# Optimization experiments

Measured on AMD Instinct MI355X. Metric: run time of the kernel, lower is better.

The kernel has to match this reference:

```python
import jax, jax.numpy as jnp
import numpy as np

N = 50000   # nodes
E = 800000  # edges (avg degree 16)
IN = 128
H = 128
OUT = 16
BN_EPS = 1e-5


def _uniform(key, shape, fan_in):
    s = 1.0 / np.sqrt(fan_in)
    return jax.random.uniform(key, shape, jnp.float32, -s, s)


def setup_inputs() -> dict:
    key = jax.random.key(0)
    ks = jax.random.split(key, 12)
    x = jax.random.normal(ks[0], (N, IN), jnp.float32)
    edge_index = jax.random.randint(ks[1], (2, E), 0, N, dtype=jnp.int64)
    # SAGEConv layer 1: lin_l (with bias) on aggregated neighbors, lin_r (no bias) on root
    Wl1 = _uniform(ks[2], (H, IN), IN)
    bl1 = _uniform(ks[3], (H,), IN)
    Wr1 = _uniform(ks[4], (H, IN), IN)
    # SAGEConv layer 2
    Wl2 = _uniform(ks[5], (OUT, H), H)
    bl2 = _uniform(ks[6], (OUT,), H)
    Wr2 = _uniform(ks[7], (OUT, H), H)
    # BatchNorm1d(H) affine params
    gamma = jnp.ones((H,), jnp.float32)
    beta = jnp.zeros((H,), jnp.float32)
    # PReLU single shared slope
    a = jnp.array(0.25, jnp.float32)
    return {"x": x, "edge_index": edge_index, "Wl1": Wl1, "bl1": bl1, "Wr1": Wr1,
            "Wl2": Wl2, "bl2": bl2, "Wr2": Wr2, "gamma": gamma, "beta": beta, "a": a}


def sage_conv(x, src, dst, Wl, bl, Wr):
    # mean-aggregate source features at destination nodes
    msg = x[src]                                              # [E, F] gather
    summ = jax.ops.segment_sum(msg, dst, num_segments=N)      # [N, F] scatter-add
    cnt = jax.ops.segment_sum(jnp.ones((src.shape[0],), x.dtype), dst, num_segments=N)
    agg = summ / jnp.clip(cnt, 1.0)[:, None]
    return agg @ Wl.T + bl + x @ Wr.T


def reference(x, edge_index, Wl1, bl1, Wr1, Wl2, bl2, Wr2, gamma, beta, a):
    src, dst = edge_index[0], edge_index[1]
    # layer 1: SAGEConv -> BatchNorm (batch stats) -> PReLU -> residual
    h = sage_conv(x, src, dst, Wl1, bl1, Wr1)
    mean = h.mean(axis=0)
    var = h.var(axis=0)  # biased, as in torch BN training
    h = gamma * (h - mean) / jnp.sqrt(var + BN_EPS) + beta
    h = jnp.where(h >= 0, h, a * h)  # PReLU (shared slope)
    h = h + x  # residual (hidden == in)
    # layer 2 + log_softmax over classes
    out = sage_conv(h, src, dst, Wl2, bl2, Wr2)
    return jax.nn.log_softmax(out, axis=1)
```

## Files before the change

### kernel.cpp

```cpp
#include <hip/hip_runtime.h>

#define NNODES 50000
#define EEDGES 800000
#define FIN 128
#define FH 128
#define FOUT 16
#define BN_EPS 1e-5f
#define NBIN 391
#define CAP 4096
#define PCH 2048
#define NPB 391
#define NTILES 1563
#define PACKBLKS 3143

typedef short bf16x8 __attribute__((ext_vector_type(8)));
typedef float f32x4 __attribute__((ext_vector_type(4)));

__device__ inline unsigned short tobf16(float f) {
    unsigned int u = __float_as_uint(f);
    u += 0x7fffu + ((u >> 16) & 1u);
    return (unsigned short)(u >> 16);
}
__device__ inline float frombf16(unsigned short h) {
    return __uint_as_float(((unsigned int)h) << 16);
}
__device__ inline unsigned packbf(float f0, float f1) {
    return (unsigned)tobf16(f0) | ((unsigned)tobf16(f1) << 16);
}
__device__ inline float lo16(unsigned u) { return __uint_as_float(u << 16); }
__device__ inline float hi16(unsigned u) { return __uint_as_float(u & 0xffff0000u); }

__global__ void zero_kernel(int* __restrict__ p) {
    for (int i = threadIdx.x; i < 647; i += 256) p[i] = 0;
}

__global__ void part_pack_kernel(const int* __restrict__ src, const int* __restrict__ dst,
                                 int* __restrict__ binFill, unsigned int* __restrict__ edgeBin,
                                 const float* __restrict__ x,
                                 const float* __restrict__ Wl1, const float* __restrict__ Wr1,
                                 const float* __restrict__ Wl2, const float* __restrict__ Wr2,
                                 unsigned short* __restrict__ xb, unsigned short* __restrict__ wb) {
    __shared__ int hist[NBIN];
    __shared__ int runBase[NBIN];
    __shared__ int runFill[NBIN];
    int t = threadIdx.x;
    if (blockIdx.x < NPB) {
        for (int i = t; i < NBIN; i += 256) { hist[i] = 0; runFill[i] = 0; }
        __syncthreads();
        int e0 = blockIdx.x * PCH;
        for (int i = 0; i < PCH / 256; ++i) {
            int e = e0 + i * 256 + t;
            if (e < EEDGES) atomicAdd(&hist[dst[e] >> 7], 1);
        }
        __syncthreads();
        for (int i = t; i < NBIN; i += 256) {
            int c = hist[i];
            if (c) runBase[i] = atomicAdd(&binFill[i], c);
        }
        __syncthreads();
        for (int i = 0; i < PCH / 256; ++i) {
            int e = e0 + i * 256 + t;
            if (e < EEDGES) {
                int d = dst[e];
                int b = d >> 7;
                int off = runBase[b] + atomicAdd(&runFill[b], 1);
                if (off < CAP)
                    edgeBin[(size_t)b * CAP + off] = ((unsigned)(d & 127) << 17) | (unsigned)src[e];
            }
        }
    } else {
        int tt = (blockIdx.x - NPB) * 256 + t;
        int base = tt * 8;
        const float* srcp;
        unsigned short* dstp;
        int off;
        if (base < NNODES * FIN) {
            srcp = x; off = base; dstp = xb + base;
        } else {
            int w = base - NNODES * FIN;
            if (w >= 36864) return;
            dstp = wb + w;
            if (w < 16384)      { srcp = Wl1; off = w; }
            else if (w < 32768) { srcp = Wr1; off = w - 16384; }
            else if (w < 34816) { srcp = Wl2; off = w - 32768; }
            else                { srcp = Wr2; off = w - 34816; }
        }
        float4 f0 = *reinterpret_cast<const float4*>(srcp + off);
        float4 f1 = *reinterpret_cast<const float4*>(srcp + off + 4);
        uint4 r;
        r.x = packbf(f0.x, f0.y);
        r.y = packbf(f0.z, f0.w);
        r.z = packbf(f1.x, f1.y);
        r.w = packbf(f1.z, f1.w);
        *reinterpret_cast<uint4*>(dstp) = r;
    }
}

__global__ void bucket_fused_kernel(const unsigned int* __restrict__ edgeBin,
                                    const int* __restrict__ binFill,
                                    int* __restrict__ srcSorted,
                                    int* __restrict__ rowstart) {
    __shared__ unsigned eb[CAP];
    __shared__ int cnt[128];
    __shared__ int sc[128];
    __shared__ int wp[128];
    __shared__ int wsum[4];
    int b = blockIdx.x;
    int t = threadIdx.x;

    int contrib = 0;
    if (t < NBIN && t < b) contrib += binFill[t];
    int t2 = t + 256;
    if (t2 < NBIN && t2 < b) contrib += binFill[t2];
    for (int off = 32; off; off >>= 1) contrib += __shfl_down(contrib, off, 64);
    if ((t & 63) == 0) wsum[t >> 6] = contrib;
    if (t < 128) cnt[t] = 0;
    __syncthreads();
    int binOffB = wsum[0] + wsum[1] + wsum[2] + wsum[3];

    int n = min(binFill[b], CAP);
    for (int k = t; k < n; k += 256) {
        unsigned c = edgeBin[(size_t)b * CAP + k];
        eb[k] = c;
        atomicAdd(&cnt[c >> 17], 1);
    }
    __syncthreads();

    if (t < 128) sc[t] = cnt[t];
    __syncthreads();
    for (int off = 1; off < 128; off <<= 1) {
        int v = (t < 128 && t >= off) ? sc[t - off] : 0;
        __syncthreads();
        if (t < 128) sc[t] += v;
        __syncthreads();
    }
    if (t < 128) {
        int node = b * 128 + t;
        int rs = binOffB + sc[t] - cnt[t];
        wp[t] = rs;
        if (node < NNODES) rowstart[node] = rs;
    }
    if (b == 0 && t == 128) rowstart[NNODES] = EEDGES;
    __syncthreads();

    for (int k = t; k < n; k += 256) {
        unsigned c = eb[k];
        int p = atomicAdd(&wp[c >> 17], 1);
        srcSorted[p] = (int)(c & 0x1FFFF);
    }
}

__global__ void gather_bf16(const unsigned short* __restrict__ feat,
                            const int* __restrict__ rowstart,
                            const int* __restrict__ srcSorted,
                            unsigned short* __restrict__ aggout) {
    int tid = threadIdx.x;
    int i = blockIdx.x * 4 + (tid >> 6);
    int j = tid & 63;
    const unsigned int* fp = (const unsigned int*)feat;
    int k0 = rowstart[i], k1 = rowstart[i + 1];
    float a0 = 0.0f, a1 = 0.0f;
    int k = k0;
    for (; k + 8 <= k1; k += 8) {
        int s0 = srcSorted[k],     s1 = srcSorted[k + 1], s2 = srcSorted[k + 2], s3 = srcSorted[k + 3];
        int s4 = srcSorted[k + 4], s5 = srcSorted[k + 5], s6 = srcSorted[k + 6], s7 = srcSorted[k + 7];
        unsigned int u0 = fp[(size_t)s0 * 64 + j];
        unsigned int u1 = fp[(size_t)s1 * 64 + j];
        unsigned int u2 = fp[(size_t)s2 * 64 + j];
        unsigned int u3 = fp[(size_t)s3 * 64 + j];
        unsigned int u4 = fp[(size_t)s4 * 64 + j];
        unsigned int u5 = fp[(size_t)s5 * 64 + j];
        unsigned int u6 = fp[(size_t)s6 * 64 + j];
        unsigned int u7 = fp[(size_t)s7 * 64 + j];
        a0 += lo16(u0) + lo16(u1) + lo16(u2) + lo16(u3) + lo16(u4) + lo16(u5) + lo16(u6) + lo16(u7);
        a1 += hi16(u0) + hi16(u1) + hi16(u2) + hi16(u3) + hi16(u4) + hi16(u5) + hi16(u6) + hi16(u7);
    }
    for (; k + 4 <= k1; k += 4) {
        int s0 = srcSorted[k], s1 = srcSorted[k + 1], s2 = srcSorted[k + 2], s3 = srcSorted[k + 3];
        unsigned int u0 = fp[(size_t)s0 * 64 + j];
        unsigned int u1 = fp[(size_t)s1 * 64 + j];
        unsigned int u2 = fp[(size_t)s2 * 64 + j];
        unsigned int u3 = fp[(size_t)s3 * 64 + j];
        a0 += lo16(u0) + lo16(u1) + lo16(u2) + lo16(u3);
        a1 += hi16(u0) + hi16(u1) + hi16(u2) + hi16(u3);
    }
    for (; k < k1; ++k) {
        unsigned int u = fp[(size_t)srcSorted[k] * 64 + j];
        a0 += lo16(u);
        a1 += hi16(u);
    }
    float inv = 1.0f / (float)max(k1 - k0, 1);
    ((unsigned int*)aggout)[(size_t)i * 64 + j] = packbf(a0 * inv, a1 * inv);
}

__global__ void __launch_bounds__(256, 2)
lin1_persist(const unsigned short* __restrict__ aggb,
             const unsigned short* __restrict__ xb,
             const unsigned short* __restrict__ wl,
             const unsigned short* __restrict__ wr,
             const float* __restrict__ bias,
             unsigned short* __restrict__ hb,
             float* __restrict__ bnsum, float* __restrict__ bnsq) {
    __shared__ float bps[128];
    __shared__ float bpq[128];
    int tid = threadIdx.x;
    if (tid < 128) { bps[tid] = 0.0f; bpq[tid] = 0.0f; }
    __syncthreads();
    int wave = tid >> 6;
    int lane = tid & 63;
    int c = wave & 1;
    int rsub = wave >> 1;
    int lrow = lane & 15;
    int kg = lane >> 4;

    bf16x8 wlF[4][4], wrF[4][4];
    #pragma unroll
    for (int nf = 0; nf < 4; ++nf) {
        #pragma unroll
        for (int ks = 0; ks < 4; ++ks) {
            wlF[nf][ks] = *(const bf16x8*)(wl + (size_t)(c * 64 + nf * 16 + lrow) * 128 + ks * 32 + kg * 8);
            wrF[nf][ks] = *(const bf16x8*)(wr + (size_t)(c * 64 + nf * 16 + lrow) * 128 + ks * 32 + kg * 8);
        }
    }
    float bias_v[4];
    #pragma unroll
    for (int nf = 0; nf < 4; ++nf) bias_v[nf] = bias[c * 64 + nf * 16 + lrow];

    for (int tIt = blockIdx.x; tIt < NTILES; tIt += gridDim.x) {
        int rowA = tIt * 32 + rsub * 16 + lrow;
        int arow = min(rowA, NNODES - 1);
        bf16x8 aA[4], aX[4];
        #pragma unroll
        for (int ks = 0; ks < 4; ++ks) {
            aA[ks] = *(const bf16x8*)(aggb + (size_t)arow * 128 + ks * 32 + kg * 8);
            aX[ks] = *(const bf16x8*)(xb + (size_t)arow * 128 + ks * 32 + kg * 8);
        }
        f32x4 acc[4] = {};
        #pragma unroll
        for (int ks = 0; ks < 4; ++ks) {
            #pragma unroll
            for (int nf = 0; nf < 4; ++nf) {
                acc[nf] = __builtin_amdgcn_mfma_f32_16x16x32_bf16(aA[ks], wlF[nf][ks], acc[nf], 0, 0, 0);
                acc[nf] = __builtin_amdgcn_mfma_f32_16x16x32_bf16(aX[ks], wrF[nf][ks], acc[nf], 0, 0, 0);
            }
        }
        #pragma unroll
        for (int nf = 0; nf < 4; ++nf) {
            float s = 0.0f, q = 0.0f;
            #pragma unroll
            for (int rr = 0; rr < 4; ++rr) {
                int row = tIt * 32 + rsub * 16 + kg * 4 + rr;
                if (row < NNODES) {
                    unsigned short hv = tobf16(acc[nf][rr] + bias_v[nf]);
                    float vr = frombf16(hv);
                    hb[(size_t)row * 128 + c * 64 + nf * 16 + lrow] = hv;
                    s += vr; q += vr * vr;
                }
            }
            s += __shfl_xor(s, 16); s += __shfl_xor(s, 32);
            q += __shfl_xor(q, 16); q += __shfl_xor(q, 32);
            if (lane < 16) {
                atomicAdd(&bps[c * 64 + nf * 16 + lane], s);
                atomicAdd(&bpq[c * 64 + nf * 16 + lane], q);
            }
        }
    }
    __syncthreads();
    if (tid < 128) {
        atomicAdd(&bnsum[tid], bps[tid]);
        atomicAdd(&bnsq[tid], bpq[tid]);
    }
}

__global__ void bn_lin2a_kernel(unsigned short* __restrict__ hb,
                                const unsigned short* __restrict__ xb,
                                const float* __restrict__ gamma, const float* __restrict__ beta,
                                const float* __restrict__ aptr,
                                const float* __restrict__ bnsum, const float* __restrict__ bnsq,
                                const unsigned short* __restrict__ wl,
                                unsigned short* __restrict__ y2) {
    __shared__ float scs[128];
    __shared__ float shs[128];
    int tid = threadIdx.x;
    if (tid < 128) {
        const float invN = 1.0f / (float)NNODES;
        float mean = bnsum[tid] * invN;
        float var = bnsq[tid] * invN - mean * mean;
        float istd = rsqrtf(var + BN_EPS);
        float sc = gamma[tid] * istd;
        scs[tid] = sc;
        shs[tid] = beta[tid] - mean * sc;
    }
    __syncthreads();
    float aP = aptr[0];
    int wave = tid >> 6;
    int lane = tid & 63;
    int row0 = blockIdx.x * 64 + wave * 16;
    int lrow = lane & 15;
    int kg = lane >> 4;
    int rowA = row0 + lrow;
    int arow = min(rowA, NNODES - 1);
    f32x4 acc = {};
    #pragma unroll
    for (int ks = 0; ks < 4; ++ks) {
        bf16x8 hv = *(const bf16x8*)(hb + (size_t)arow * 128 + ks * 32 + kg * 8);
        bf16x8 xv = *(const bf16x8*)(xb + (size_t)arow * 128 + ks * 32 + kg * 8);
        bf16x8 nv;
        #pragma unroll
        for (int e = 0; e < 8; ++e) {
            int f = ks * 32 + kg * 8 + e;
            float v = frombf16((unsigned short)hv[e]) * scs[f] + shs[f];
            v = (v >= 0.0f) ? v : aP * v;
            v += frombf16((unsigned short)xv[e]);
            nv[e] = (short)tobf16(v);
        }
        if (rowA < NNODES)
            *(bf16x8*)(hb + (size_t)arow * 128 + ks * 32 + kg * 8) = nv;
        bf16x8 b = *(const bf16x8*)(wl + (size_t)lrow * 128 + ks * 32 + kg * 8);
        acc = __builtin_amdgcn_mfma_f32_16x16x32_bf16(nv, b, acc, 0, 0, 0);
    }
    #pragma unroll
    for (int r = 0; r < 4; ++r) {
        int row = row0 + kg * 4 + r;
        if (row < NNODES)
            y2[(size_t)row * 16 + lrow] = tobf16(acc[r]);
    }
}

__global__ void gather16_lin2b_kernel(const unsigned short* __restrict__ y2,
                                      const int* __restrict__ rowstart,
                                      const int* __restrict__ srcSorted,
                                      const unsigned short* __restrict__ hb,
                                      const unsigned short* __restrict__ wr,
                                      const float* __restrict__ bias,
                                      float* __restrict__ out) {
    __shared__ float agg[64][16];
    int t = threadIdx.x;
    int w = t >> 6;
    int lane = t & 63;
    int e = lane >> 3;
    int j = lane & 7;
    const unsigned int* yp = (const unsigned int*)y2;
    int nodeBase = blockIdx.x * 64;

    for (int it = 0; it < 16; ++it) {
        int i = nodeBase + w * 16 + it;
        int ic = min(i, NNODES - 1);
        int k0 = rowstart[ic], k1 = rowstart[ic + 1];
        float a0 = 0.0f, a1 = 0.0f;
        for (int k = k0; k < k1; k += 8) {
            int kk = k + e;
            if (kk < k1) {
                unsigned u = yp[(size_t)srcSorted[kk] * 8 + j];
                a0 += lo16(u);
                a1 += hi16(u);
            }
        }
        a0 += __shfl_xor(a0, 8);  a1 += __shfl_xor(a1, 8);
        a0 += __shfl_xor(a0, 16); a1 += __shfl_xor(a1, 16);
        a0 += __shfl_xor(a0, 32); a1 += __shfl_xor(a1, 32);
        if (e == 0) {
            float inv = 1.0f / (float)max(k1 - k0, 1);
            agg[w * 16 + it][2 * j]     = a0 * inv;
            agg[w * 16 + it][2 * j + 1] = a1 * inv;
        }
    }
    __syncthreads();

    int lrow = lane & 15;
    int kg = lane >> 4;
    int row0 = nodeBase + w * 16;
    int arow = min(row0 + lrow, NNODES - 1);
    f32x4 acc = {};
    #pragma unroll
    for (int ks = 0; ks < 4; ++ks) {
        bf16x8 a = *(const bf16x8*)(hb + (size_t)arow * 128 + ks * 32 + kg * 8);
        bf16x8 b = *(const bf16x8*)(wr + (size_t)lrow * 128 + ks * 32 + kg * 8);
        acc = __builtin_amdgcn_mfma_f32_16x16x32_bf16(a, b, acc, 0, 0, 0);
    }
    float bl = bias[lrow];
    #pragma unroll
    for (int r = 0; r < 4; ++r) {
        int row = row0 + kg * 4 + r;
        int lr = w * 16 + kg * 4 + r;
        float v = acc[r] + bl + agg[lr][lrow];
        float m = v;
        for (int s = 1; s < 16; s <<= 1) m = fmaxf(m, __shfl_xor(m, s, 16));
        float ex = expf(v - m);
        float se = ex;
        for (int s = 1; s < 16; s <<= 1) se += __shfl_xor(se, s, 16);
        if (row < NNODES)
            out[(size_t)row * FOUT + lrow] = v - m - logf(se);
    }
}

extern "C" void kernel_launch(void* const* d_in, const int* in_sizes, int n_in,
                              void* d_out, int out_size, void* d_ws, size_t ws_size,
                              hipStream_t stream) {
    const float* x    = (const float*)d_in[0];
    const int*   ei   = (const int*)d_in[1];
    const int*   src  = ei;
    const int*   dst  = ei + EEDGES;
    const float* Wl1  = (const float*)d_in[2];
    const float* bl1  = (const float*)d_in[3];
    const float* Wr1  = (const float*)d_in[4];
    const float* Wl2  = (const float*)d_in[5];
    const float* bl2  = (const float*)d_in[6];
    const float* Wr2  = (const float*)d_in[7];
    const float* gamma= (const float*)d_in[8];
    const float* beta = (const float*)d_in[9];
    const float* a    = (const float*)d_in[10];
    float* out = (float*)d_out;

    char* W = (char*)d_ws;
    unsigned short* xb    = (unsigned short*)(W + 0);
    unsigned short* hb    = (unsigned short*)(W + 12800000);
    unsigned int*  edgeBin= (unsigned int*)(W + 25600000);
    unsigned short* aggb  = (unsigned short*)(W + 25600000);
    unsigned short* y2b   = (unsigned short*)(W + 25600000);
    unsigned short* wb    = (unsigned short*)(W + 38400000);
    int* binFill  = (int*)(W + 38473728);
    float* bnsum  = (float*)(W + 38475292);
    float* bnsq   = (float*)(W + 38475804);
    int* rowstart = (int*)(W + 38678072);
    int* srcSorted= (int*)(W + 38878076);

    unsigned short* wl1b = wb;
    unsigned short* wr1b = wb + 16384;
    unsigned short* wl2b = wb + 32768;
    unsigned short* wr2b = wb + 34816;

    zero_kernel<<<1, 256, 0, stream>>>(binFill);

    part_pack_kernel<<<NPB + PACKBLKS, 256, 0, stream>>>(src, dst, binFill, edgeBin,
                                                         x, Wl1, Wr1, Wl2, Wr2, xb, wb);
    bucket_fused_kernel<<<NBIN, 256, 0, stream>>>(edgeBin, binFill, srcSorted, rowstart);

    gather_bf16<<<NNODES / 4, 256, 0, stream>>>(xb, rowstart, srcSorted, aggb);
    lin1_persist<<<512, 256, 0, stream>>>(aggb, xb, wl1b, wr1b, bl1, hb, bnsum, bnsq);

    bn_lin2a_kernel<<<782, 256, 0, stream>>>(hb, xb, gamma, beta, a, bnsum, bnsq, wl2b, y2b);

    gather16_lin2b_kernel<<<782, 256, 0, stream>>>(y2b, rowstart, srcSorted, hb, wr2b, bl2, out);
}
```

Measured before the change: 146.4 us.

## Split layer-2 gather from lin2b, widen gather loads, use per-wave partition histograms

The layer-2 kernel is split into a one-node-per-wave gather kernel with many more blocks, plus a separate MFMA lin2b kernel that reads the aggregated bf16 rows from workspace. The layer-1 gather now loads 8 bytes per lane, with the two half-waves taking alternate edges and merging through a shuffle. The edge partitioner uses per-wave shared histograms to cut LDS atomic contention. In exchange there is one extra launch and a small bf16 round-trip of the aggregate through memory, which adds rounding.

```diff
diff --git a/kernel.cpp b/kernel.cpp
--- a/kernel.cpp
+++ b/kernel.cpp
@@ -40,22 +40,28 @@
                                  const float* __restrict__ Wl1, const float* __restrict__ Wr1,
                                  const float* __restrict__ Wl2, const float* __restrict__ Wr2,
                                  unsigned short* __restrict__ xb, unsigned short* __restrict__ wb) {
-    __shared__ int hist[NBIN];
-    __shared__ int runBase[NBIN];
-    __shared__ int runFill[NBIN];
+    __shared__ int hist4[4][NBIN];
     int t = threadIdx.x;
     if (blockIdx.x < NPB) {
-        for (int i = t; i < NBIN; i += 256) { hist[i] = 0; runFill[i] = 0; }
+        int w = t >> 6;
+        for (int i = t; i < NBIN; i += 256) {
+            hist4[0][i] = 0; hist4[1][i] = 0; hist4[2][i] = 0; hist4[3][i] = 0;
+        }
         __syncthreads();
         int e0 = blockIdx.x * PCH;
         for (int i = 0; i < PCH / 256; ++i) {
             int e = e0 + i * 256 + t;
-            if (e < EEDGES) atomicAdd(&hist[dst[e] >> 7], 1);
+            if (e < EEDGES) atomicAdd(&hist4[w][dst[e] >> 7], 1);
         }
         __syncthreads();
         for (int i = t; i < NBIN; i += 256) {
-            int c = hist[i];
-            if (c) runBase[i] = atomicAdd(&binFill[i], c);
+            int h0 = hist4[0][i], h1 = hist4[1][i], h2 = hist4[2][i], h3 = hist4[3][i];
+            int c = h0 + h1 + h2 + h3;
+            int base = c ? atomicAdd(&binFill[i], c) : 0;
+            hist4[0][i] = base;
+            hist4[1][i] = base + h0;
+            hist4[2][i] = base + h0 + h1;
+            hist4[3][i] = base + h0 + h1 + h2;
         }
         __syncthreads();
         for (int i = 0; i < PCH / 256; ++i) {
@@ -63,7 +69,7 @@
             if (e < EEDGES) {
                 int d = dst[e];
                 int b = d >> 7;
-                int off = runBase[b] + atomicAdd(&runFill[b], 1);
+                int off = atomicAdd(&hist4[w][b], 1);
                 if (off < CAP)
                     edgeBin[(size_t)b * CAP + off] = ((unsigned)(d & 127) << 17) | (unsigned)src[e];
             }
@@ -77,13 +83,13 @@
         if (base < NNODES * FIN) {
             srcp = x; off = base; dstp = xb + base;
         } else {
-            int w = base - NNODES * FIN;
-            if (w >= 36864) return;
-            dstp = wb + w;
-            if (w < 16384)      { srcp = Wl1; off = w; }
-            else if (w < 32768) { srcp = Wr1; off = w - 16384; }
-            else if (w < 34816) { srcp = Wl2; off = w - 32768; }
-            else                { srcp = Wr2; off = w - 34816; }
+            int w2 = base - NNODES * FIN;
+            if (w2 >= 36864) return;
+            dstp = wb + w2;
+            if (w2 < 16384)      { srcp = Wl1; off = w2; }
+            else if (w2 < 32768) { srcp = Wr1; off = w2 - 16384; }
+            else if (w2 < 34816) { srcp = Wl2; off = w2 - 32768; }
+            else                 { srcp = Wr2; off = w2 - 34816; }
         }
         float4 f0 = *reinterpret_cast<const float4*>(srcp + off);
         float4 f1 = *reinterpret_cast<const float4*>(srcp + off + 4);
@@ -156,41 +162,46 @@
                             unsigned short* __restrict__ aggout) {
     int tid = threadIdx.x;
     int i = blockIdx.x * 4 + (tid >> 6);
-    int j = tid & 63;
-    const unsigned int* fp = (const unsigned int*)feat;
+    int lane = tid & 63;
+    int half = lane >> 5;
+    int j = lane & 31;
+    const uint2* fp = (const uint2*)feat;
     int k0 = rowstart[i], k1 = rowstart[i + 1];
-    float a0 = 0.0f, a1 = 0.0f;
+    float a0 = 0.0f, a1 = 0.0f, a2 = 0.0f, a3 = 0.0f;
     int k = k0;
     for (; k + 8 <= k1; k += 8) {
-        int s0 = srcSorted[k],     s1 = srcSorted[k + 1], s2 = srcSorted[k + 2], s3 = srcSorted[k + 3];
-        int s4 = srcSorted[k + 4], s5 = srcSorted[k + 5], s6 = srcSorted[k + 6], s7 = srcSorted[k + 7];
-        unsigned int u0 = fp[(size_t)s0 * 64 + j];
-        unsigned int u1 = fp[(size_t)s1 * 64 + j];
-        unsigned int u2 = fp[(size_t)s2 * 64 + j];
-        unsigned int u3 = fp[(size_t)s3 * 64 + j];
-        unsigned int u4 = fp[(size_t)s4 * 64 + j];
-        unsigned int u5 = fp[(size_t)s5 * 64 + j];
-        unsigned int u6 = fp[(size_t)s6 * 64 + j];
-        unsigned int u7 = fp[(size_t)s7 * 64 + j];
-        a0 += lo16(u0) + lo16(u1) + lo16(u2) + lo16(u3) + lo16(u4) + lo16(u5) + lo16(u6) + lo16(u7);
-        a1 += hi16(u0) + hi16(u1) + hi16(u2) + hi16(u3) + hi16(u4) + hi16(u5) + hi16(u6) + hi16(u7);
-    }
-    for (; k + 4 <= k1; k += 4) {
-        int s0 = srcSorted[k], s1 = srcSorted[k + 1], s2 = srcSorted[k + 2], s3 = srcSorted[k + 3];
-        unsigned int u0 = fp[(size_t)s0 * 64 + j];
-        unsigned int u1 = fp[(size_t)s1 * 64 + j];
-        unsigned int u2 = fp[(size_t)s2 * 64 + j];
-        unsigned int u3 = fp[(size_t)s3 * 64 + j];
-        a0 += lo16(u0) + lo16(u1) + lo16(u2) + lo16(u3);
-        a1 += hi16(u0) + hi16(u1) + hi16(u2) + hi16(u3);
-    }
-    for (; k < k1; ++k) {
-        unsigned int u = fp[(size_t)srcSorted[k] * 64 + j];
-        a0 += lo16(u);
-        a1 += hi16(u);
-    }
-    float inv = 1.0f / (float)max(k1 - k0, 1);
-    ((unsigned int*)aggout)[(size_t)i * 64 + j] = packbf(a0 * inv, a1 * inv);
+        int sA = srcSorted[k + half];
+        int sB = srcSorted[k + 2 + half];
+        int sC = srcSorted[k + 4 + half];
+        int sD = srcSorted[k + 6 + half];
+        uint2 uA = fp[(size_t)sA * 32 + j];
+        uint2 uB = fp[(size_t)sB * 32 + j];
+        uint2 uC = fp[(size_t)sC * 32 + j];
+        uint2 uD = fp[(size_t)sD * 32 + j];
+        a0 += lo16(uA.x) + lo16(uB.x) + lo16(uC.x) + lo16(uD.x);
+        a1 += hi16(uA.x) + hi16(uB.x) + hi16(uC.x) + hi16(uD.x);
+        a2 += lo16(uA.y) + lo16(uB.y) + lo16(uC.y) + lo16(uD.y);
+        a3 += hi16(uA.y) + hi16(uB.y) + hi16(uC.y) + hi16(uD.y);
+    }
+    for (; k + 2 <= k1; k += 2) {
+        int s = srcSorted[k + half];
+        uint2 u = fp[(size_t)s * 32 + j];
+        a0 += lo16(u.x); a1 += hi16(u.x); a2 += lo16(u.y); a3 += hi16(u.y);
+    }
+    if (k < k1 && half == 0) {
+        int s = srcSorted[k];
+        uint2 u = fp[(size_t)s * 32 + j];
+        a0 += lo16(u.x); a1 += hi16(u.x); a2 += lo16(u.y); a3 += hi16(u.y);
+    }
+    a0 += __shfl_xor(a0, 32); a1 += __shfl_xor(a1, 32);
+    a2 += __shfl_xor(a2, 32); a3 += __shfl_xor(a3, 32);
+    if (half == 0) {
+        float inv = 1.0f / (float)max(k1 - k0, 1);
+        uint2 r;
+        r.x = packbf(a0 * inv, a1 * inv);
+        r.y = packbf(a2 * inv, a3 * inv);
+        ((uint2*)aggout)[(size_t)i * 32 + j] = r;
+    }
 }
 
 __global__ void __launch_bounds__(256, 2)
@@ -327,49 +338,45 @@
     }
 }
 
-__global__ void gather16_lin2b_kernel(const unsigned short* __restrict__ y2,
-                                      const int* __restrict__ rowstart,
-                                      const int* __restrict__ srcSorted,
-                                      const unsigned short* __restrict__ hb,
-                                      const unsigned short* __restrict__ wr,
-                                      const float* __restrict__ bias,
-                                      float* __restrict__ out) {
-    __shared__ float agg[64][16];
-    int t = threadIdx.x;
-    int w = t >> 6;
-    int lane = t & 63;
+__global__ void gather16_kernel(const unsigned short* __restrict__ y2,
+                                const int* __restrict__ rowstart,
+                                const int* __restrict__ srcSorted,
+                                unsigned short* __restrict__ agg2) {
+    int tid = threadIdx.x;
+    int i = blockIdx.x * 4 + (tid >> 6);
+    int lane = tid & 63;
     int e = lane >> 3;
     int j = lane & 7;
     const unsigned int* yp = (const unsigned int*)y2;
-    int nodeBase = blockIdx.x * 64;
-
-    for (int it = 0; it < 16; ++it) {
-        int i = nodeBase + w * 16 + it;
-        int ic = min(i, NNODES - 1);
-        int k0 = rowstart[ic], k1 = rowstart[ic + 1];
-        float a0 = 0.0f, a1 = 0.0f;
-        for (int k = k0; k < k1; k += 8) {
-            int kk = k + e;
-            if (kk < k1) {
-                unsigned u = yp[(size_t)srcSorted[kk] * 8 + j];
-                a0 += lo16(u);
-                a1 += hi16(u);
-            }
-        }
-        a0 += __shfl_xor(a0, 8);  a1 += __shfl_xor(a1, 8);
-        a0 += __shfl_xor(a0, 16); a1 += __shfl_xor(a1, 16);
-        a0 += __shfl_xor(a0, 32); a1 += __shfl_xor(a1, 32);
-        if (e == 0) {
-            float inv = 1.0f / (float)max(k1 - k0, 1);
-            agg[w * 16 + it][2 * j]     = a0 * inv;
-            agg[w * 16 + it][2 * j + 1] = a1 * inv;
-        }
-    }
-    __syncthreads();
-
+    int k0 = rowstart[i], k1 = rowstart[i + 1];
+    float a0 = 0.0f, a1 = 0.0f;
+    for (int k = k0; k < k1; k += 8) {
+        int kk = k + e;
+        if (kk < k1) {
+            unsigned u = yp[(size_t)srcSorted[kk] * 8 + j];
+            a0 += lo16(u);
+            a1 += hi16(u);
+        }
+    }
+    a0 += __shfl_xor(a0, 8);  a1 += __shfl_xor(a1, 8);
+    a0 += __shfl_xor(a0, 16); a1 += __shfl_xor(a1, 16);
+    a0 += __shfl_xor(a0, 32); a1 += __shfl_xor(a1, 32);
+    if (e == 0) {
+        float inv = 1.0f / (float)max(k1 - k0, 1);
+        ((unsigned int*)agg2)[(size_t)i * 8 + j] = packbf(a0 * inv, a1 * inv);
+    }
+}
+
+__global__ void lin2b_kernel(const unsigned short* __restrict__ agg2,
+                             const unsigned short* __restrict__ hb,
+                             const unsigned short* __restrict__ wr,
+                             const float* __restrict__ bias,
+                             float* __restrict__ out) {
+    int wave = threadIdx.x >> 6;
+    int lane = threadIdx.x & 63;
+    int row0 = blockIdx.x * 64 + wave * 16;
     int lrow = lane & 15;
     int kg = lane >> 4;
-    int row0 = nodeBase + w * 16;
     int arow = min(row0 + lrow, NNODES - 1);
     f32x4 acc = {};
     #pragma unroll
@@ -382,8 +389,8 @@
     #pragma unroll
     for (int r = 0; r < 4; ++r) {
         int row = row0 + kg * 4 + r;
-        int lr = w * 16 + kg * 4 + r;
-        float v = acc[r] + bl + agg[lr][lrow];
+        int rowc = min(row, NNODES - 1);
+        float v = acc[r] + bl + frombf16(agg2[(size_t)rowc * 16 + lrow]);
         float m = v;
         for (int s = 1; s < 16; s <<= 1) m = fmaxf(m, __shfl_xor(m, s, 16));
         float ex = expf(v - m);
@@ -418,6 +425,7 @@
     unsigned int*  edgeBin= (unsigned int*)(W + 25600000);
     unsigned short* aggb  = (unsigned short*)(W + 25600000);
     unsigned short* y2b   = (unsigned short*)(W + 25600000);
+    unsigned short* agg2b = (unsigned short*)(W + 27200000);
     unsigned short* wb    = (unsigned short*)(W + 38400000);
     int* binFill  = (int*)(W + 38473728);
     float* bnsum  = (float*)(W + 38475292);
@@ -441,5 +449,6 @@
 
     bn_lin2a_kernel<<<782, 256, 0, stream>>>(hb, xb, gamma, beta, a, bnsum, bnsq, wl2b, y2b);
 
-    gather16_lin2b_kernel<<<782, 256, 0, stream>>>(y2b, rowstart, srcSorted, hb, wr2b, bl2, out);
-}
+    gather16_kernel<<<NNODES / 4, 256, 0, stream>>>(y2b, rowstart, srcSorted, agg2b);
+    lin2b_kernel<<<782, 256, 0, stream>>>(agg2b, hb, wr2b, bl2, out);
+}
```

After: 138.6 us, median of 2. 5.3% less time.
